# Kernel tuning notes

Measured on AMD Instinct MI355X. Metric: run time of the kernel, lower is better.

The kernel has to match this reference:

```python
import jax, jax.numpy as jnp
import numpy as np


def layer_norm(x, gamma, beta, eps=1e-6):
    # Torch module uses unbiased std (ddof=1) and divides by (std + eps)
    mean = x.mean(-1, keepdims=True)
    std = jnp.std(x, axis=-1, keepdims=True, ddof=1)
    return gamma * (x - mean) / (std + eps) + beta


def gelu_erf(x):
    return 0.5 * x * (1.0 + jax.lax.erf(x / jnp.sqrt(jnp.asarray(2.0, x.dtype))))


def setup_inputs() -> dict:
    B, S, D, H, F = 32, 512, 1024, 16, 4096
    key = jax.random.key(0)
    ks = jax.random.split(key, 16)
    w = lambda k, shp: (jax.random.normal(k, shp, jnp.float32) * 0.02)
    return {
        "x": jax.random.normal(ks[0], (B, S, D), jnp.float32),
        "mask": jax.random.randint(ks[1], (B, S), 0, 2).astype(jnp.int32),
        "adj": jax.random.normal(ks[2], (B, 1, S, S), jnp.float32) * 0.1,
        "num_head": H,
        "Wq": w(ks[3], (D, D)), "bq": jnp.zeros((D,), jnp.float32),
        "Wk": w(ks[4], (D, D)), "bk": jnp.zeros((D,), jnp.float32),
        "Wv": w(ks[5], (D, D)), "bv": jnp.zeros((D,), jnp.float32),
        "Wo": w(ks[6], (D, D)), "bo": jnp.zeros((D,), jnp.float32),
        "W1": w(ks[7], (D, F)), "b1": jnp.zeros((F,), jnp.float32),
        "W2": w(ks[8], (F, D)), "b2": jnp.zeros((D,), jnp.float32),
        "gamma": jnp.ones((D,), jnp.float32),
        "beta": jnp.zeros((D,), jnp.float32),
    }


def reference(x, mask, adj, num_head, Wq, bq, Wk, bk, Wv, bv, Wo, bo,
              W1, b1, W2, b2, gamma, beta):
    B, S, D = x.shape
    H = num_head
    dk = D // H
    split = lambda t: t.reshape(B, S, H, dk).transpose(0, 2, 1, 3)  # [B,H,S,dk]
    q = split(x @ Wq + bq)
    k = split(x @ Wk + bk)
    v = split(x @ Wv + bv)
    scores = jnp.einsum('bhqd,bhkd->bhqk', q, k) / np.float32(np.sqrt(dk))
    m = mask[:, None, None, :].astype(x.dtype)  # [B,1,1,S]
    scores = scores + m * jnp.asarray(-1e9, x.dtype) + adj
    attn = jax.nn.softmax(scores, axis=-1)
    ctx = jnp.einsum('bhqk,bhkd->bhqd', attn, v)
    ctx = ctx.transpose(0, 2, 1, 3).reshape(B, S, D)
    attn_out = ctx @ Wo + bo  # dropout is identity at eval
    out1 = layer_norm(x + attn_out, gamma, beta)
    ffn = gelu_erf(out1 @ W1 + b1) @ W2 + b2
    return layer_norm(out1 + ffn, gamma, beta)
```

## Files before the change

kernel.cpp:

```cpp
#include <hip/hip_runtime.h>
#include <stdint.h>
#include <math.h>

typedef unsigned short u16;
typedef __attribute__((ext_vector_type(8))) __bf16 bf16x8;
typedef __attribute__((ext_vector_type(4))) float f32x4;
typedef __attribute__((ext_vector_type(4))) unsigned short u16x4;

__device__ __forceinline__ float b2f(u16 u) {
    unsigned int i = ((unsigned int)u) << 16;
    float f; __builtin_memcpy(&f, &i, 4); return f;
}
__device__ __forceinline__ u16 f2b(float f) {
    unsigned int i; __builtin_memcpy(&i, &f, 4);
    i = (i + 0x7FFFu + ((i >> 16) & 1u)) >> 16;
    return (u16)i;
}
__device__ __forceinline__ bf16x8 ld8_cvt(const float* p) {
    float4 f0 = *(const float4*)p, f1 = *(const float4*)(p + 4);
    u16 t[8] = {f2b(f0.x), f2b(f0.y), f2b(f0.z), f2b(f0.w),
                f2b(f1.x), f2b(f1.y), f2b(f1.z), f2b(f1.w)};
    bf16x8 r; __builtin_memcpy(&r, t, 16); return r;
}

__device__ __forceinline__ void glds16(const u16* g, u16* l) {
    __builtin_amdgcn_global_load_lds(
        (const __attribute__((address_space(1))) void*)g,
        (__attribute__((address_space(3))) void*)l, 16, 0, 0);
}

__global__ __launch_bounds__(256) void transpose_f32_bf16(
    const float* __restrict__ in, u16* __restrict__ out, int R, int C)
{
    __shared__ float t[32][33];
    int bx = blockIdx.x * 32, by = blockIdx.y * 32;
    int x = threadIdx.x, y = threadIdx.y;
    #pragma unroll
    for (int j = 0; j < 32; j += 8)
        t[y + j][x] = in[(size_t)(by + y + j) * C + bx + x];
    __syncthreads();
    #pragma unroll
    for (int j = 0; j < 32; j += 8)
        out[(size_t)(bx + y + j) * R + by + x] = f2b(t[x][y + j]);
}

__global__ __launch_bounds__(256) void cvt_f32_bf16(
    const float* __restrict__ in, u16* __restrict__ out)
{
    size_t i = ((size_t)blockIdx.x * 256 + threadIdx.x) * 8;
    *(bf16x8*)(out + i) = ld8_cvt(in + i);
}

template<int EPI>
__global__ __launch_bounds__(512, 2) void gemm256(
    const u16* __restrict__ A, const u16* __restrict__ Bt, int N, int K,
    u16* __restrict__ C, const float* __restrict__ bias,
    u16* __restrict__ qo, u16* __restrict__ ko, u16* __restrict__ vo,
    const float* __restrict__ bq, const float* __restrict__ bk,
    const float* __restrict__ bv)
{
    __shared__ __align__(16) u16 Asm[2][256 * 32];
    __shared__ __align__(16) u16 Bsm[2][256 * 32];
    const int tid  = threadIdx.x;
    const int lane = tid & 63, wave = tid >> 6;
    const int lrow = lane & 15, quad = lane >> 4;
    const int wm = wave >> 2, wn = wave & 3;
    const int bm = blockIdx.x * 256, bn = blockIdx.y * 256;

    const int srow = tid >> 2;
    const int skolS = (((tid & 3) ^ ((tid >> 3) & 3)) * 8);
    const u16* gA = A  + (size_t)(bm + srow) * K + skolS;
    const u16* gB = Bt + (size_t)(bn + srow) * K + skolS;
    const size_t rstep = (size_t)128 * K;

    const int xq = quad ^ ((lrow >> 1) & 3);

    f32x4 acc[8][4] = {};

#define STAGE256(T, BUF) do {                                              \
        glds16(gA + (size_t)(T) * 32,         &Asm[BUF][(size_t)tid * 8]); \
        glds16(gA + (size_t)(T) * 32 + rstep, &Asm[BUF][((size_t)tid + 512) * 8]); \
        glds16(gB + (size_t)(T) * 32,         &Bsm[BUF][(size_t)tid * 8]); \
        glds16(gB + (size_t)(T) * 32 + rstep, &Bsm[BUF][((size_t)tid + 512) * 8]); \
    } while (0)

    const int ntile = K >> 5;
    STAGE256(0, 0);
    STAGE256(1, 1);
    asm volatile("s_waitcnt vmcnt(4)" ::: "memory");
    __builtin_amdgcn_s_barrier();
    __builtin_amdgcn_sched_barrier(0);

    for (int t = 0; t < ntile; ++t) {
        const int cur = t & 1;
        bf16x8 af[8], bfr[4];
        #pragma unroll
        for (int mt = 0; mt < 8; mt++)
            af[mt] = *(const bf16x8*)&Asm[cur][(wm * 128 + mt * 16 + lrow) * 32 + xq * 8];
        #pragma unroll
        for (int nt = 0; nt < 4; nt++)
            bfr[nt] = *(const bf16x8*)&Bsm[cur][(wn * 64 + nt * 16 + lrow) * 32 + xq * 8];
        #pragma unroll
        for (int mt = 0; mt < 8; mt++)
            #pragma unroll
            for (int nt = 0; nt < 4; nt++)
                acc[mt][nt] = __builtin_amdgcn_mfma_f32_16x16x32_bf16(
                    af[mt], bfr[nt], acc[mt][nt], 0, 0, 0);

        if (t + 1 < ntile) {
            __builtin_amdgcn_sched_barrier(0);
            __builtin_amdgcn_s_barrier();
            if (t + 2 < ntile) {
                STAGE256(t + 2, cur);
                asm volatile("s_waitcnt vmcnt(4)" ::: "memory");
            } else {
                asm volatile("s_waitcnt vmcnt(0)" ::: "memory");
            }
            __builtin_amdgcn_s_barrier();
            __builtin_amdgcn_sched_barrier(0);
        }
    }
#undef STAGE256

    __syncthreads();
    constexpr int STR = (EPI == 2) ? 64 : 68;
    u16* stg = ((u16*)Asm) + wave * 1152;

    const int colb = bn + wn * 64;
    float bval[4];
    u16* dstp = nullptr;
    int hh = 0, bb = 0;
    if (EPI == 2) {
        int mat = colb >> 10, dcol0 = colb & 1023;
        hh = dcol0 >> 6;
        const float* bp = (mat == 0) ? bq : ((mat == 1) ? bk : bv);
        #pragma unroll
        for (int nt = 0; nt < 4; nt++) bval[nt] = bp[dcol0 + nt * 16 + lrow];
        dstp = (mat == 0) ? qo : ((mat == 1) ? ko : vo);
        bb = (bm + wm * 128) >> 9;
    } else {
        #pragma unroll
        for (int nt = 0; nt < 4; nt++) bval[nt] = bias[colb + nt * 16 + lrow];
    }

    #pragma unroll
    for (int mt = 0; mt < 8; mt++) {
        const int row0 = bm + wm * 128 + mt * 16;
        #pragma unroll
        for (int nt = 0; nt < 4; nt++)
            #pragma unroll
            for (int r = 0; r < 4; r++) {
                float v = acc[mt][nt][r] + bval[nt];
                if (EPI == 1) v = 0.5f * v * (1.0f + erff(v * 0.70710678118654752f));
                stg[(quad * 4 + r) * STR + nt * 16 + lrow] = f2b(v);
            }
        if (EPI == 2) {
            int s0 = row0 & 511;
            size_t base = (((size_t)(bb * 16 + hh)) * 512 + s0) * 64;
            #pragma unroll
            for (int i = 0; i < 2; i++)
                *(bf16x8*)(dstp + base + (size_t)(i * 64 + lane) * 8) =
                    *(const bf16x8*)&stg[(i * 64 + lane) * 8];
        } else {
            #pragma unroll
            for (int i = 0; i < 2; i++) {
                int rl = i * 8 + (lane >> 3);
                *(bf16x8*)(C + (size_t)(row0 + rl) * N + colb + (lane & 7) * 8) =
                    *(const bf16x8*)&stg[rl * STR + (lane & 7) * 8];
            }
        }
    }
}

template<int EPI, int BN>
__global__ __launch_bounds__(256) void gemm_bt(
    const u16* __restrict__ A, const u16* __restrict__ Bt, int N, int K,
    u16* __restrict__ C, const float* __restrict__ bias,
    u16* __restrict__ qo, u16* __restrict__ ko, u16* __restrict__ vo,
    const float* __restrict__ bq, const float* __restrict__ bk,
    const float* __restrict__ bv)
{
    __shared__ __align__(16) u16 Asm[2][128 * 32];
    __shared__ __align__(16) u16 Bsm[2][BN * 32];
    const int tid  = threadIdx.x;
    const int lane = tid & 63;
    const int wave = tid >> 6;
    const int lrow = lane & 15, quad = lane >> 4;
    const int bm = blockIdx.x * 128, bn = blockIdx.y * BN;

    const int srow = tid >> 2;
    const int skolS = (((tid & 3) ^ ((tid >> 3) & 3)) * 8);
    const u16* gA0 = A  + (size_t)(bm + srow) * K + skolS;
    const u16* gA1 = gA0 + (size_t)64 * K;
    const u16* gB0 = Bt + (size_t)(bn + srow) * K + skolS;
    const u16* gB1 = gB0 + (size_t)64 * K;

    const int xq = quad ^ ((lrow >> 1) & 3);

    const int wm = wave >> 1, wn = wave & 1;
    constexpr int NT = (BN == 128) ? 4 : 2;
    f32x4 acc[4][NT] = {};

    glds16(gA0, &Asm[0][(size_t)tid * 8]);
    glds16(gA1, &Asm[0][((size_t)tid + 256) * 8]);
    if constexpr (BN == 128) glds16(gB1, &Bsm[0][((size_t)tid + 256) * 8]);
    glds16(gB0, &Bsm[0][(size_t)tid * 8]);

    int cur = 0;
    for (int kt = 0; kt < K; kt += 32) {
        const int nxt = kt + 32;
        if (nxt < K) {
            glds16(gA0 + nxt, &Asm[cur ^ 1][(size_t)tid * 8]);
            glds16(gA1 + nxt, &Asm[cur ^ 1][((size_t)tid + 256) * 8]);
            if constexpr (BN == 128)
                glds16(gB1 + nxt, &Bsm[cur ^ 1][((size_t)tid + 256) * 8]);
            glds16(gB0 + nxt, &Bsm[cur ^ 1][(size_t)tid * 8]);
            if constexpr (BN == 128)
                asm volatile("s_waitcnt vmcnt(4)" ::: "memory");
            else
                asm volatile("s_waitcnt vmcnt(3)" ::: "memory");
        } else {
            asm volatile("s_waitcnt vmcnt(0)" ::: "memory");
        }
        __builtin_amdgcn_s_barrier();
        __builtin_amdgcn_sched_barrier(0);

        bf16x8 af[4], bfr[NT];
        #pragma unroll
        for (int mt = 0; mt < 4; mt++)
            af[mt] = *(const bf16x8*)&Asm[cur][(wm * 64 + mt * 16 + lrow) * 32 + xq * 8];
        #pragma unroll
        for (int nt = 0; nt < NT; nt++)
            bfr[nt] = *(const bf16x8*)&Bsm[cur][(wn * (BN / 2) + nt * 16 + lrow) * 32 + xq * 8];
        #pragma unroll
        for (int mt = 0; mt < 4; mt++)
            #pragma unroll
            for (int nt = 0; nt < NT; nt++)
                acc[mt][nt] = __builtin_amdgcn_mfma_f32_16x16x32_bf16(
                    af[mt], bfr[nt], acc[mt][nt], 0, 0, 0);

        __builtin_amdgcn_sched_barrier(0);
        __builtin_amdgcn_s_barrier();
        cur ^= 1;
    }

    #pragma unroll
    for (int nt = 0; nt < NT; nt++) {
        int col = bn + wn * (BN / 2) + nt * 16 + lrow;
        int mat = 0, hh = 0, dd = 0;
        float bval;
        if (EPI == 2) {
            mat  = col >> 10; int dcol = col & 1023;
            hh = dcol >> 6;   dd = dcol & 63;
            const float* bp = (mat == 0) ? bq : ((mat == 1) ? bk : bv);
            bval = bp[dcol];
        } else {
            bval = bias[col];
        }
        #pragma unroll
        for (int mt = 0; mt < 4; mt++) {
            #pragma unroll
            for (int r = 0; r < 4; r++) {
                int row = bm + wm * 64 + mt * 16 + quad * 4 + r;
                float v = acc[mt][nt][r] + bval;
                if (EPI == 1) v = 0.5f * v * (1.0f + erff(v * 0.70710678118654752f));
                if (EPI == 2) {
                    int b = row >> 9, s = row & 511;
                    u16* dst = (mat == 0) ? qo : ((mat == 1) ? ko : vo);
                    dst[(((size_t)(b * 16 + hh)) * 512 + s) * 64 + dd] = f2b(v);
                } else {
                    C[(size_t)row * N + col] = f2b(v);
                }
            }
        }
    }
}

__global__ __launch_bounds__(256) void attn_kernel(
    const u16* __restrict__ Q, const u16* __restrict__ Kb, const u16* __restrict__ Vb,
    const float* __restrict__ adj, const int* __restrict__ mask, u16* __restrict__ ctx)
{
    const int S = 512, H = 16;
    __shared__ __align__(16) u16 Ksm[2][32 * 64];
    __shared__ __align__(16) u16 Vt [2][64 * 32];
    __shared__ __align__(16) u16 Psm[4][16 * 32];

    int tid = threadIdx.x, lane = tid & 63, wave = tid >> 6;
    int lrow = lane & 15, quad = lane >> 4;

    int orig = (blockIdx.z * 16 + blockIdx.y) * 8 + blockIdx.x;
    int b  = orig & 7;
    int h  = (orig >> 3) & 15;
    int qt = orig >> 7;

    size_t headoff = ((size_t)(b * H + h)) * S * 64;
    const u16* qp = Q + headoff;
    const u16* kp = Kb + headoff;
    const u16* vp = Vb + headoff;
    const float* adjb = adj + (size_t)b * S * S;
    const int* maskb = mask + b * S;
    int q0 = qt * 64 + wave * 16;

    bf16x8 qf0 = *(const bf16x8*)(qp + (size_t)(q0 + lrow) * 64 + quad * 8);
    bf16x8 qf1 = *(const bf16x8*)(qp + (size_t)(q0 + lrow) * 64 + 32 + quad * 8);

    float m_run[4] = {-1e30f, -1e30f, -1e30f, -1e30f};
    float l_run[4] = {0.f, 0.f, 0.f, 0.f};
    f32x4 o[4] = {};

    int str = tid >> 3;
    int stc = (tid & 7) * 8;
    int stcS = (((tid & 7) ^ ((tid >> 3) & 7)) * 8);
    const int xk = lrow & 7;

    glds16(kp + (size_t)str * 64 + stcS, &Ksm[0][str * 64 + stc]);
    bf16x8 vcur = *(const bf16x8*)(vp + (size_t)str * 64 + stc);
    __syncthreads();

    int cur = 0;
    for (int kt = 0; kt < S; kt += 32) {
        const int nxt = kt + 32;
        bf16x8 vnxt;
        if (nxt < S) {
            glds16(kp + (size_t)(nxt + str) * 64 + stcS, &Ksm[cur ^ 1][str * 64 + stc]);
            vnxt = *(const bf16x8*)(vp + (size_t)(nxt + str) * 64 + stc);
        }
        {
            const u16* tv = (const u16*)&vcur;
            #pragma unroll
            for (int j = 0; j < 8; j++) Vt[cur][(stc + j) * 32 + str] = tv[j];
        }
        float adjv[2][4];
        #pragma unroll
        for (int f = 0; f < 2; f++)
            #pragma unroll
            for (int r = 0; r < 4; r++)
                adjv[f][r] = adjb[(size_t)(q0 + quad * 4 + r) * S + kt + f * 16 + lrow];

        f32x4 sc[2];
        #pragma unroll
        for (int f = 0; f < 2; f++) {
            f32x4 cf = {};
            bf16x8 kf0 = *(const bf16x8*)&Ksm[cur][(f * 16 + lrow) * 64 + (quad ^ xk) * 8];
            bf16x8 kf1 = *(const bf16x8*)&Ksm[cur][(f * 16 + lrow) * 64 + ((quad + 4) ^ xk) * 8];
            cf = __builtin_amdgcn_mfma_f32_16x16x32_bf16(qf0, kf0, cf, 0, 0, 0);
            cf = __builtin_amdgcn_mfma_f32_16x16x32_bf16(qf1, kf1, cf, 0, 0, 0);
            int key = kt + f * 16 + lrow;
            float mterm = maskb[key] ? -1e9f : 0.0f;
            #pragma unroll
            for (int r = 0; r < 4; r++)
                sc[f][r] = cf[r] * 0.125f + mterm + adjv[f][r];
        }

        float mx[4], al[4], sm[4];
        #pragma unroll
        for (int r = 0; r < 4; r++) mx[r] = fmaxf(sc[0][r], sc[1][r]);
        #pragma unroll
        for (int mk = 1; mk < 16; mk <<= 1)
            #pragma unroll
            for (int r = 0; r < 4; r++) mx[r] = fmaxf(mx[r], __shfl_xor(mx[r], mk));
        #pragma unroll
        for (int r = 0; r < 4; r++) {
            float mn = fmaxf(m_run[r], mx[r]);
            al[r] = __expf(fminf(m_run[r] - mn, 0.f));
            m_run[r] = mn;
        }
        #pragma unroll
        for (int f = 0; f < 2; f++)
            #pragma unroll
            for (int r = 0; r < 4; r++)
                sc[f][r] = __expf(fminf(sc[f][r] - m_run[r], 0.f));
        #pragma unroll
        for (int r = 0; r < 4; r++) sm[r] = sc[0][r] + sc[1][r];
        #pragma unroll
        for (int mk = 1; mk < 16; mk <<= 1)
            #pragma unroll
            for (int r = 0; r < 4; r++) sm[r] += __shfl_xor(sm[r], mk);
        #pragma unroll
        for (int r = 0; r < 4; r++) l_run[r] = l_run[r] * al[r] + sm[r];
        #pragma unroll
        for (int nt = 0; nt < 4; nt++)
            #pragma unroll
            for (int r = 0; r < 4; r++) o[nt][r] *= al[r];

        #pragma unroll
        for (int f = 0; f < 2; f++)
            #pragma unroll
            for (int r = 0; r < 4; r++)
                Psm[wave][(quad * 4 + r) * 32 + f * 16 + lrow] = f2b(sc[f][r]);
        bf16x8 pa = *(const bf16x8*)&Psm[wave][lrow * 32 + quad * 8];

        __syncthreads();
        #pragma unroll
        for (int nt = 0; nt < 4; nt++) {
            bf16x8 vf = *(const bf16x8*)&Vt[cur][(nt * 16 + lrow) * 32 + quad * 8];
            o[nt] = __builtin_amdgcn_mfma_f32_16x16x32_bf16(pa, vf, o[nt], 0, 0, 0);
        }
        if (nxt < S) vcur = vnxt;
        cur ^= 1;
    }

    #pragma unroll
    for (int nt = 0; nt < 4; nt++)
        #pragma unroll
        for (int r = 0; r < 4; r++) {
            int qrow = q0 + quad * 4 + r;
            ctx[((size_t)b * 512 + qrow) * 1024 + h * 64 + nt * 16 + lrow] =
                f2b(o[nt][r] / l_run[r]);
        }
}

template<int MODE>
__global__ __launch_bounds__(256) void add_ln(
    const void* __restrict__ Xv, const void* __restrict__ Yv,
    const float* __restrict__ gamma, const float* __restrict__ beta,
    void* __restrict__ outv)
{
    const int D = 1024;
    int row = blockIdx.x, tid = threadIdx.x;
    int lane = tid & 63, wave = tid >> 6;
    size_t base = (size_t)row * D + tid * 4;

    float x[4];
    if (MODE == 0) {
        float4 xf = *(const float4*)((const float*)Xv + base);
        u16x4  uy = *(const u16x4*)((const u16*)Yv + base);
        x[0] = xf.x + b2f(uy[0]); x[1] = xf.y + b2f(uy[1]);
        x[2] = xf.z + b2f(uy[2]); x[3] = xf.w + b2f(uy[3]);
    } else {
        u16x4 ux = *(const u16x4*)((const u16*)Xv + base);
        u16x4 uy = *(const u16x4*)((const u16*)Yv + base);
        #pragma unroll
        for (int j = 0; j < 4; j++) x[j] = b2f(ux[j]) + b2f(uy[j]);
    }

    float s = x[0] + x[1] + x[2] + x[3];
    #pragma unroll
    for (int mk = 1; mk < 64; mk <<= 1) s += __shfl_xor(s, mk);
    __shared__ float red[8];
    if (lane == 0) red[wave] = s;
    __syncthreads();
    float mean = (red[0] + red[1] + red[2] + red[3]) * (1.0f / 1024.0f);

    float c[4], q = 0.f;
    #pragma unroll
    for (int j = 0; j < 4; j++) { c[j] = x[j] - mean; q += c[j] * c[j]; }
    #pragma unroll
    for (int mk = 1; mk < 64; mk <<= 1) q += __shfl_xor(q, mk);
    if (lane == 0) red[4 + wave] = q;
    __syncthreads();
    float var = (red[4] + red[5] + red[6] + red[7]) * (1.0f / 1023.0f);
    float inv = 1.0f / (sqrtf(var) + 1e-6f);

    float4 g4 = *(const float4*)(gamma + tid * 4);
    float4 b4 = *(const float4*)(beta + tid * 4);
    float gv[4] = {g4.x, g4.y, g4.z, g4.w};
    float bv[4] = {b4.x, b4.y, b4.z, b4.w};
    if (MODE == 0) {
        u16x4 ov;
        #pragma unroll
        for (int j = 0; j < 4; j++) ov[j] = f2b(gv[j] * c[j] * inv + bv[j]);
        *(u16x4*)((u16*)outv + base) = ov;
    } else {
        float4 ov;
        ov.x = gv[0] * c[0] * inv + bv[0];
        ov.y = gv[1] * c[1] * inv + bv[1];
        ov.z = gv[2] * c[2] * inv + bv[2];
        ov.w = gv[3] * c[3] * inv + bv[3];
        *(float4*)((float*)outv + base) = ov;
    }
}

extern "C" void kernel_launch(void* const* d_in, const int* in_sizes, int n_in,
                              void* d_out, int out_size, void* d_ws, size_t ws_size,
                              hipStream_t stream)
{
    const float* x    = (const float*)d_in[0];
    const int*   mask = (const int*)d_in[1];
    const float* adj  = (const float*)d_in[2];
    const float* Wq = (const float*)d_in[4];  const float* bq = (const float*)d_in[5];
    const float* Wk = (const float*)d_in[6];  const float* bk = (const float*)d_in[7];
    const float* Wv = (const float*)d_in[8];  const float* bv = (const float*)d_in[9];
    const float* Wo = (const float*)d_in[10]; const float* bo = (const float*)d_in[11];
    const float* W1 = (const float*)d_in[12]; const float* b1 = (const float*)d_in[13];
    const float* W2 = (const float*)d_in[14]; const float* b2 = (const float*)d_in[15];
    const float* gamma = (const float*)d_in[16];
    const float* beta  = (const float*)d_in[17];
    float* out = (float*)d_out;

    const size_t MB = 1024ull * 1024;
    char* w = (char*)d_ws;
    u16* Wqkv_t = (u16*)(w + 0 * MB);
    u16* Wo_t   = (u16*)(w + 6 * MB);
    u16* W1_t   = (u16*)(w + 8 * MB);
    u16* W2_t   = (u16*)(w + 16 * MB);
    u16* out1   = (u16*)(w + 24 * MB);
    u16* qg     = (u16*)(w + 56 * MB);
    u16* kg     = (u16*)(w + 64 * MB);
    u16* vg     = (u16*)(w + 72 * MB);
    u16* ctxg   = (u16*)(w + 80 * MB);
    u16* aog    = (u16*)(w + 88 * MB);
    u16* hid    = (u16*)(w + 56 * MB);
    u16* ffn    = (u16*)(w + 88 * MB);

    dim3 tb(32, 8);
    transpose_f32_bf16<<<dim3(32, 32),  tb, 0, stream>>>(Wq, Wqkv_t,                1024, 1024);
    transpose_f32_bf16<<<dim3(32, 32),  tb, 0, stream>>>(Wk, Wqkv_t + 1024ull*1024, 1024, 1024);
    transpose_f32_bf16<<<dim3(32, 32),  tb, 0, stream>>>(Wv, Wqkv_t + 2048ull*1024, 1024, 1024);
    transpose_f32_bf16<<<dim3(32, 32),  tb, 0, stream>>>(Wo, Wo_t,                  1024, 1024);
    transpose_f32_bf16<<<dim3(128, 32), tb, 0, stream>>>(W1, W1_t,                  1024, 4096);
    transpose_f32_bf16<<<dim3(32, 128), tb, 0, stream>>>(W2, W2_t,                  4096, 1024);

    for (int g = 0; g < 4; g++) {
        const float* xg = x + (size_t)g * 4096 * 1024;
        cvt_f32_bf16<<<2048, 256, 0, stream>>>(xg, aog);
        gemm256<2><<<dim3(16, 12), 512, 0, stream>>>(aog, Wqkv_t, 3072, 1024,
            nullptr, nullptr, qg, kg, vg, bq, bk, bv);
        attn_kernel<<<dim3(8, 16, 8), 256, 0, stream>>>(qg, kg, vg,
            adj + (size_t)g * 8 * 512 * 512, mask + g * 8 * 512, ctxg);
        gemm_bt<0, 64><<<dim3(32, 16), 256, 0, stream>>>(ctxg, Wo_t, 1024, 1024,
            aog, bo, nullptr, nullptr, nullptr, nullptr, nullptr, nullptr);
        add_ln<0><<<4096, 256, 0, stream>>>(xg, aog, gamma, beta,
            out1 + (size_t)g * 4096 * 1024);
    }

    for (int c = 0; c < 4; c++) {
        const u16* o1c = out1 + (size_t)c * 4096 * 1024;
        gemm256<1><<<dim3(16, 16), 512, 0, stream>>>(o1c, W1_t, 4096, 1024,
            hid, b1, nullptr, nullptr, nullptr, nullptr, nullptr, nullptr);
        gemm_bt<0, 64><<<dim3(32, 16), 256, 0, stream>>>(hid, W2_t, 1024, 4096,
            ffn, b2, nullptr, nullptr, nullptr, nullptr, nullptr, nullptr);
        add_ln<1><<<4096, 256, 0, stream>>>(o1c, ffn, gamma, beta,
            out + (size_t)c * 4096 * 1024);
    }
}
```

Measured before the change: 1.272 ms.

## Triple-buffer LDS tiles in both GEMM kernels for deeper prefetch

Both GEMM kernels move from double to triple buffered shared-memory tiles and prefetch three K-tiles ahead, using rotating buffer indices and adjusted vmcnt waits. The goal is to hide more global-load latency behind MFMA work. The cost is 50% more LDS per block, which can reduce how many blocks fit on a CU, especially for the 256x256 kernel.

```diff
diff --git a/kernel.cpp b/kernel.cpp
--- a/kernel.cpp
+++ b/kernel.cpp
@@ -59,8 +59,8 @@
     const float* __restrict__ bq, const float* __restrict__ bk,
     const float* __restrict__ bv)
 {
-    __shared__ __align__(16) u16 Asm[2][256 * 32];
-    __shared__ __align__(16) u16 Bsm[2][256 * 32];
+    __shared__ __align__(16) u16 Asm[3][256 * 32];
+    __shared__ __align__(16) u16 Bsm[3][256 * 32];
     const int tid  = threadIdx.x;
     const int lane = tid & 63, wave = tid >> 6;
     const int lrow = lane & 15, quad = lane >> 4;
@@ -87,12 +87,13 @@
     const int ntile = K >> 5;
     STAGE256(0, 0);
     STAGE256(1, 1);
-    asm volatile("s_waitcnt vmcnt(4)" ::: "memory");
+    STAGE256(2, 2);
+    asm volatile("s_waitcnt vmcnt(8)" ::: "memory");
     __builtin_amdgcn_s_barrier();
     __builtin_amdgcn_sched_barrier(0);
 
+    int cur = 0;
     for (int t = 0; t < ntile; ++t) {
-        const int cur = t & 1;
         bf16x8 af[8], bfr[4];
         #pragma unroll
         for (int mt = 0; mt < 8; mt++)
@@ -110,8 +111,10 @@
         if (t + 1 < ntile) {
             __builtin_amdgcn_sched_barrier(0);
             __builtin_amdgcn_s_barrier();
-            if (t + 2 < ntile) {
-                STAGE256(t + 2, cur);
+            if (t + 3 < ntile) {
+                STAGE256(t + 3, cur);
+                asm volatile("s_waitcnt vmcnt(8)" ::: "memory");
+            } else if (t + 3 == ntile) {
                 asm volatile("s_waitcnt vmcnt(4)" ::: "memory");
             } else {
                 asm volatile("s_waitcnt vmcnt(0)" ::: "memory");
@@ -119,6 +122,7 @@
             __builtin_amdgcn_s_barrier();
             __builtin_amdgcn_sched_barrier(0);
         }
+        cur = (cur == 2) ? 0 : cur + 1;
     }
 #undef STAGE256
 
@@ -180,8 +184,8 @@
     const float* __restrict__ bq, const float* __restrict__ bk,
     const float* __restrict__ bv)
 {
-    __shared__ __align__(16) u16 Asm[2][128 * 32];
-    __shared__ __align__(16) u16 Bsm[2][BN * 32];
+    __shared__ __align__(16) u16 Asm[3][128 * 32];
+    __shared__ __align__(16) u16 Bsm[3][BN * 32];
     const int tid  = threadIdx.x;
     const int lane = tid & 63;
     const int wave = tid >> 6;
@@ -201,30 +205,27 @@
     constexpr int NT = (BN == 128) ? 4 : 2;
     f32x4 acc[4][NT] = {};
 
-    glds16(gA0, &Asm[0][(size_t)tid * 8]);
-    glds16(gA1, &Asm[0][((size_t)tid + 256) * 8]);
-    if constexpr (BN == 128) glds16(gB1, &Bsm[0][((size_t)tid + 256) * 8]);
-    glds16(gB0, &Bsm[0][(size_t)tid * 8]);
+#define STAGEBT(T, BUF) do {                                                   \
+        glds16(gA0 + (size_t)(T) * 32, &Asm[BUF][(size_t)tid * 8]);            \
+        glds16(gA1 + (size_t)(T) * 32, &Asm[BUF][((size_t)tid + 256) * 8]);    \
+        if constexpr (BN == 128)                                               \
+            glds16(gB1 + (size_t)(T) * 32, &Bsm[BUF][((size_t)tid + 256) * 8]);\
+        glds16(gB0 + (size_t)(T) * 32, &Bsm[BUF][(size_t)tid * 8]);            \
+    } while (0)
+
+    const int ntile = K >> 5;
+    STAGEBT(0, 0);
+    STAGEBT(1, 1);
+    STAGEBT(2, 2);
+    if constexpr (BN == 128)
+        asm volatile("s_waitcnt vmcnt(8)" ::: "memory");
+    else
+        asm volatile("s_waitcnt vmcnt(6)" ::: "memory");
+    __builtin_amdgcn_s_barrier();
+    __builtin_amdgcn_sched_barrier(0);
 
     int cur = 0;
-    for (int kt = 0; kt < K; kt += 32) {
-        const int nxt = kt + 32;
-        if (nxt < K) {
-            glds16(gA0 + nxt, &Asm[cur ^ 1][(size_t)tid * 8]);
-            glds16(gA1 + nxt, &Asm[cur ^ 1][((size_t)tid + 256) * 8]);
-            if constexpr (BN == 128)
-                glds16(gB1 + nxt, &Bsm[cur ^ 1][((size_t)tid + 256) * 8]);
-            glds16(gB0 + nxt, &Bsm[cur ^ 1][(size_t)tid * 8]);
-            if constexpr (BN == 128)
-                asm volatile("s_waitcnt vmcnt(4)" ::: "memory");
-            else
-                asm volatile("s_waitcnt vmcnt(3)" ::: "memory");
-        } else {
-            asm volatile("s_waitcnt vmcnt(0)" ::: "memory");
-        }
-        __builtin_amdgcn_s_barrier();
-        __builtin_amdgcn_sched_barrier(0);
-
+    for (int t = 0; t < ntile; ++t) {
         bf16x8 af[4], bfr[NT];
         #pragma unroll
         for (int mt = 0; mt < 4; mt++)
@@ -239,10 +240,29 @@
                 acc[mt][nt] = __builtin_amdgcn_mfma_f32_16x16x32_bf16(
                     af[mt], bfr[nt], acc[mt][nt], 0, 0, 0);
 
-        __builtin_amdgcn_sched_barrier(0);
-        __builtin_amdgcn_s_barrier();
-        cur ^= 1;
-    }
+        if (t + 1 < ntile) {
+            __builtin_amdgcn_sched_barrier(0);
+            __builtin_amdgcn_s_barrier();
+            if (t + 3 < ntile) {
+                STAGEBT(t + 3, cur);
+                if constexpr (BN == 128)
+                    asm volatile("s_waitcnt vmcnt(8)" ::: "memory");
+                else
+                    asm volatile("s_waitcnt vmcnt(6)" ::: "memory");
+            } else if (t + 3 == ntile) {
+                if constexpr (BN == 128)
+                    asm volatile("s_waitcnt vmcnt(4)" ::: "memory");
+                else
+                    asm volatile("s_waitcnt vmcnt(3)" ::: "memory");
+            } else {
+                asm volatile("s_waitcnt vmcnt(0)" ::: "memory");
+            }
+            __builtin_amdgcn_s_barrier();
+            __builtin_amdgcn_sched_barrier(0);
+        }
+        cur = (cur == 2) ? 0 : cur + 1;
+    }
+#undef STAGEBT
 
     #pragma unroll
     for (int nt = 0; nt < NT; nt++) {
```

Result: no change. 1.281 ms (+0.7%).
